# Kernel optimization log

Measured on AMD Instinct MI355X. Metric: run time of the kernel, lower is better.

Reference implementation:

```python
import jax, jax.numpy as jnp
import numpy as np

HIDDEN = 1024
EMB = HIDDEN // 2          # embedding_dim = hidden_dim // 2
NUM_OPS = 8
BATCH = 16384


def setup_inputs() -> dict:
    key = jax.random.key(0)
    ks = jax.random.split(key, 8)
    x = jax.random.normal(ks[0], (BATCH, HIDDEN), dtype=jnp.float32)
    sampled_ops = jax.random.randint(ks[1], (BATCH,), 0, NUM_OPS, dtype=jnp.int32)
    op_emb = jax.random.normal(ks[2], (NUM_OPS, EMB), dtype=jnp.float32) * 0.02
    # per-expert 2-layer MLP params (Linear stored as [in, out] for x @ W)
    s1 = 1.0 / np.sqrt(HIDDEN + EMB)
    s2 = 1.0 / np.sqrt(HIDDEN)
    W1 = jax.random.uniform(ks[3], (NUM_OPS, HIDDEN + EMB, HIDDEN), jnp.float32, -s1, s1)
    b1 = jax.random.uniform(ks[4], (NUM_OPS, HIDDEN), jnp.float32, -s1, s1)
    W2 = jax.random.uniform(ks[5], (NUM_OPS, HIDDEN, HIDDEN), jnp.float32, -s2, s2)
    b2 = jax.random.uniform(ks[6], (NUM_OPS, HIDDEN), jnp.float32, -s2, s2)
    return {"x": x, "sampled_ops": sampled_ops, "op_emb": op_emb,
            "W1": W1, "b1": b1, "W2": W2, "b2": b2}


def reference(x, sampled_ops, op_emb, W1, b1, W2, b2):
    # gather per-token operator embedding and augment input
    emb = jnp.take(op_emb, sampled_ops, axis=0)            # [B, EMB]
    x_aug = jnp.concatenate([x, emb], axis=-1)             # [B, H+EMB]
    num_ops = W1.shape[0]
    out = jnp.zeros_like(x)
    # loop over the small fixed expert set; mask-combine per token
    for o in range(num_ops):
        h = jax.nn.relu(x_aug @ W1[o] + b1[o])             # [B, H]
        y = jax.nn.relu(h @ W2[o] + b2[o])                 # [B, H]
        mask = (sampled_ops == o)[:, None]
        out = out + jnp.where(mask, y, 0.0)
    return out
```

## Files before the change

kernel.cpp:

```cpp
#include <hip/hip_runtime.h>
#include <hip/hip_bf16.h>

#define BATCH 16384
#define HID   1024
#define EMBD  512
#define NOPS  8
#define MAXT  136
#define CNTS  16

typedef __attribute__((ext_vector_type(8))) short bf16x8;
typedef __attribute__((ext_vector_type(4))) float f32x4;

__device__ __forceinline__ unsigned short f2bf(float f) {
  unsigned int u = __float_as_uint(f);
  u += 0x7FFF + ((u >> 16) & 1);
  return (unsigned short)(u >> 16);
}

__device__ __forceinline__ unsigned int pk2(float a, float b) {
  __hip_bfloat162 t = __float22bfloat162_rn(make_float2(a, b));
  return *(unsigned int*)(&t);
}

__device__ __forceinline__ void lds_load16(void* lds, const void* g) {
  __builtin_amdgcn_global_load_lds(
      (const __attribute__((address_space(1))) unsigned int*)g,
      (__attribute__((address_space(3))) unsigned int*)lds, 16, 0, 0);
}

__device__ __forceinline__ void decode_bid(int bid, int& g, int& nx) {
  g = 17 * (bid & 7) + (bid >> 6);
  nx = (bid >> 3) & 7;
}

__device__ __forceinline__ void w_prep_tile(const float* __restrict__ W,
                                            short* __restrict__ Wp,
                                            int ks, int nx, int tid) {
  int n = tid & 127, kh = tid >> 7;
  const float* src = W + (size_t)(ks * 32 + kh * 16) * 1024 + nx * 128 + n;
  float v[16];
#pragma unroll
  for (int kk = 0; kk < 16; ++kk) v[kk] = src[(size_t)kk * 1024];
  uint4 a, b;
  a.x = pk2(v[0], v[1]);  a.y = pk2(v[2], v[3]);
  a.z = pk2(v[4], v[5]);  a.w = pk2(v[6], v[7]);
  b.x = pk2(v[8], v[9]);  b.y = pk2(v[10], v[11]);
  b.z = pk2(v[12], v[13]); b.w = pk2(v[14], v[15]);
  uint4* dst = (uint4*)(Wp + (size_t)n * 32);
  dst[kh * 2] = a;
  dst[kh * 2 + 1] = b;
}

__global__ void bucket_w1_k(const int* __restrict__ ops, int* __restrict__ cnt,
                            int* __restrict__ idx, const float* __restrict__ W1,
                            short* __restrict__ W1p) {
  int bid = blockIdx.x;
  int tid = threadIdx.x;
  if (bid >= 64) {
    int b = bid - 64;
    int e = b / 384; int r = b % 384; int nx = r / 48, ks = r % 48;
    w_prep_tile(W1 + (size_t)e * 1536 * 1024,
                W1p + ((size_t)(e * 8 + nx) * 48 + ks) * 4096, ks, nx, tid);
    return;
  }
  __shared__ int wcnt[4][NOPS];
  __shared__ int wbase[4][NOPS];
  int lane = tid & 63, w = tid >> 6;
  int t = bid * 256 + tid;
  int op = ops[t];
  unsigned long long msave = 0;
#pragma unroll
  for (int o = 0; o < NOPS; ++o) {
    unsigned long long mm = __ballot(op == o);
    if (op == o) msave = mm;
    if (lane == o) wcnt[w][o] = __popcll(mm);
  }
  __syncthreads();
  if (tid < NOPS) {
    int c0 = wcnt[0][tid], c1 = wcnt[1][tid], c2 = wcnt[2][tid], c3 = wcnt[3][tid];
    int base = atomicAdd(&cnt[tid * CNTS], c0 + c1 + c2 + c3);
    wbase[0][tid] = base;
    wbase[1][tid] = base + c0;
    wbase[2][tid] = base + c0 + c1;
    wbase[3][tid] = base + c0 + c1 + c2;
  }
  __syncthreads();
  int pre = __popcll(msave & ((1ull << lane) - 1ull));
  idx[op * BATCH + wbase[w][op] + pre] = t;
}

__global__ void schedule_k(const int* __restrict__ cnt, int* __restrict__ desc,
                           int* __restrict__ ntp, int* __restrict__ idx) {
  if (threadIdx.x == 0) {
    int n = 0;
    for (int e = 0; e < NOPS; ++e) {
      int c = cnt[e * CNTS];
      for (int t = 0; t < c; t += 128) { desc[2 * n] = e; desc[2 * n + 1] = t; ++n; }
    }
    *ntp = n;
  }
  for (int e = 0; e < NOPS; ++e) {
    int c = cnt[e * CNTS];
    int cp = (c + 127) & ~127;
    for (int p = c + (int)threadIdx.x; p < cp; p += 256) idx[e * BATCH + p] = 0;
  }
}

__global__ void prep_a_k(const float* __restrict__ x, const float* __restrict__ emb,
                         const int* __restrict__ idx, const int* __restrict__ desc,
                         const int* __restrict__ ntp, short* __restrict__ Ap) {
  __shared__ int toks[128];
  int bid = blockIdx.x;
  int g = bid / 12, kx = bid % 12;
  if (g >= *ntp) return;
  int e = desc[2 * g], rs = desc[2 * g + 1];
  int tid = threadIdx.x;
  if (tid < 128) toks[tid] = idx[e * BATCH + rs + tid];
  __syncthreads();
  int r = tid >> 1, ah = tid & 1;
  int tok = toks[r];
  short* dst0 = Ap + (size_t)g * 48 * 4096;
#pragma unroll
  for (int kk = 0; kk < 4; ++kk) {
    int ks = kx * 4 + kk;
    const float* src = (ks < 32) ? (x + (size_t)tok * HID + ks * 32 + ah * 16)
                                 : (emb + e * EMBD + (ks - 32) * 32 + ah * 16);
    float4 f0 = ((const float4*)src)[0];
    float4 f1 = ((const float4*)src)[1];
    float4 f2v = ((const float4*)src)[2];
    float4 f3 = ((const float4*)src)[3];
    uint4 p0 = make_uint4(pk2(f0.x, f0.y), pk2(f0.z, f0.w), pk2(f1.x, f1.y), pk2(f1.z, f1.w));
    uint4 p1 = make_uint4(pk2(f2v.x, f2v.y), pk2(f2v.z, f2v.w), pk2(f3.x, f3.y), pk2(f3.z, f3.w));
    short* dst = dst0 + ks * 4096 + r * 32 + ah * 16;
    ((uint4*)dst)[0] = p0;
    ((uint4*)dst)[1] = p1;
  }
}

__global__ __launch_bounds__(256) void gemm1_w2_k(
    const short* __restrict__ Ap, const float* __restrict__ b1,
    const short* __restrict__ W1p, unsigned short* __restrict__ hp,
    const int* __restrict__ desc, const int* __restrict__ ntp,
    const float* __restrict__ W2, short* __restrict__ W2p) {
  int bid = blockIdx.x;
  int tid = threadIdx.x;
  if (bid >= 8 * MAXT) {
    int b = bid - 8 * MAXT;
    int e = b / 256; int r = b % 256; int nx = r / 32, ks = r % 32;
    w_prep_tile(W2 + (size_t)e * 1024 * 1024,
                W2p + ((size_t)(e * 8 + nx) * 32 + ks) * 4096, ks, nx, tid);
    return;
  }
  int g, nx;
  decode_bid(bid, g, nx);
  if (g >= *ntp) return;
  int e = desc[2 * g];

  __shared__ __align__(16) char smem[16384];
  short* lA = (short*)smem;
  short* lB = (short*)(smem + 8192);

  int lane = tid & 63, w = tid >> 6;
  int wm = w >> 1, wn = w & 1;
  int fr = lane & 15, fq = lane >> 4;

  const char* Asrc = (const char*)Ap + (size_t)g * 48 * 8192;
  const char* Bsrc = (const char*)W1p + (size_t)(e * 8 + nx) * 48 * 8192;

  f32x4 acc[4][4] = {};

  for (int ks = 0; ks < 48; ++ks) {
    const char* as = Asrc + ks * 8192;
    const char* bs = Bsrc + ks * 8192;
    lds_load16(smem + w * 1024, as + w * 1024 + lane * 16);
    lds_load16(smem + 4096 + w * 1024, as + 4096 + w * 1024 + lane * 16);
    lds_load16(smem + 8192 + w * 1024, bs + w * 1024 + lane * 16);
    lds_load16(smem + 12288 + w * 1024, bs + 4096 + w * 1024 + lane * 16);
    __syncthreads();

    bf16x8 af[4], bfr[4];
#pragma unroll
    for (int i = 0; i < 4; ++i)
      af[i] = *(const bf16x8*)&lA[(wm * 64 + i * 16 + fr) * 32 + fq * 8];
#pragma unroll
    for (int j = 0; j < 4; ++j)
      bfr[j] = *(const bf16x8*)&lB[(wn * 64 + j * 16 + fr) * 32 + fq * 8];
#pragma unroll
    for (int i = 0; i < 4; ++i)
#pragma unroll
      for (int j = 0; j < 4; ++j)
        acc[i][j] = __builtin_amdgcn_mfma_f32_16x16x32_bf16(af[i], bfr[j], acc[i][j], 0, 0, 0);
    __syncthreads();
  }

  float bias[4];
#pragma unroll
  for (int j = 0; j < 4; ++j)
    bias[j] = b1[e * HID + nx * 128 + wn * 64 + j * 16 + fr];

  unsigned short* ls = (unsigned short*)smem;
  int lr = lane >> 2;
#pragma unroll
  for (int i = 0; i < 4; ++i) {
    __syncthreads();
#pragma unroll
    for (int j = 0; j < 4; ++j)
#pragma unroll
      for (int rg = 0; rg < 4; ++rg) {
        float v = acc[i][j][rg] + bias[j];
        v = v > 0.f ? v : 0.f;
        ls[w * 1024 + (fq * 4 + rg) * 64 + j * 16 + fr] = f2bf(v);
      }
    __syncthreads();
    int R = wm * 64 + i * 16 + lr;
#pragma unroll
    for (int s = 0; s < 2; ++s) {
      int ch = (lane & 3) + s * 4;
      int ks2 = nx * 4 + wn * 2 + (ch >> 2);
      uint4 val = *(const uint4*)&ls[w * 1024 + lr * 64 + ch * 8];
      *(uint4*)(hp + ((size_t)(g * 32 + ks2) * 128 + R) * 32 + (ch & 3) * 8) = val;
    }
  }
}

__global__ __launch_bounds__(256) void gemm2_k(
    const unsigned short* __restrict__ hp, const float* __restrict__ b2,
    const short* __restrict__ W2p, float* __restrict__ out,
    const int* __restrict__ idx, const int* __restrict__ cnt,
    const int* __restrict__ desc, const int* __restrict__ ntp) {
  int g, nx;
  decode_bid(blockIdx.x, g, nx);
  if (g >= *ntp) return;
  int e = desc[2 * g], rs = desc[2 * g + 1];
  int ce = cnt[e * CNTS];

  __shared__ __align__(16) char smem[16384];
  __shared__ int toks[128];
  short* lA = (short*)smem;
  short* lB = (short*)(smem + 8192);

  int tid = threadIdx.x, lane = tid & 63, w = tid >> 6;
  int wm = w >> 1, wn = w & 1;
  int fr = lane & 15, fq = lane >> 4;

  if (tid < 128) toks[tid] = idx[e * BATCH + rs + tid];

  const char* Asrc = (const char*)hp + (size_t)g * 32 * 8192;
  const char* Bsrc = (const char*)W2p + (size_t)(e * 8 + nx) * 32 * 8192;

  f32x4 acc[4][4] = {};

  for (int ks = 0; ks < 32; ++ks) {
    const char* as = Asrc + ks * 8192;
    const char* bs = Bsrc + ks * 8192;
    lds_load16(smem + w * 1024, as + w * 1024 + lane * 16);
    lds_load16(smem + 4096 + w * 1024, as + 4096 + w * 1024 + lane * 16);
    lds_load16(smem + 8192 + w * 1024, bs + w * 1024 + lane * 16);
    lds_load16(smem + 12288 + w * 1024, bs + 4096 + w * 1024 + lane * 16);
    __syncthreads();

    bf16x8 af[4], bfr[4];
#pragma unroll
    for (int i = 0; i < 4; ++i)
      af[i] = *(const bf16x8*)&lA[(wm * 64 + i * 16 + fr) * 32 + fq * 8];
#pragma unroll
    for (int j = 0; j < 4; ++j)
      bfr[j] = *(const bf16x8*)&lB[(wn * 64 + j * 16 + fr) * 32 + fq * 8];
#pragma unroll
    for (int i = 0; i < 4; ++i)
#pragma unroll
      for (int j = 0; j < 4; ++j)
        acc[i][j] = __builtin_amdgcn_mfma_f32_16x16x32_bf16(af[i], bfr[j], acc[i][j], 0, 0, 0);
    __syncthreads();
  }

  float bias[4];
#pragma unroll
  for (int j = 0; j < 4; ++j)
    bias[j] = b2[e * HID + nx * 128 + wn * 64 + j * 16 + fr];

  float* lsf = (float*)smem;
  int lr = lane >> 2;
#pragma unroll
  for (int i = 0; i < 4; ++i) {
    __syncthreads();
#pragma unroll
    for (int j = 0; j < 4; ++j)
#pragma unroll
      for (int rg = 0; rg < 4; ++rg) {
        float v = acc[i][j][rg] + bias[j];
        lsf[w * 1024 + (fq * 4 + rg) * 64 + j * 16 + fr] = v > 0.f ? v : 0.f;
      }
    __syncthreads();
    int R = wm * 64 + i * 16 + lr;
    if (R < ce - rs) {
      float* orow = out + (size_t)toks[R] * HID + nx * 128 + wn * 64;
#pragma unroll
      for (int s = 0; s < 4; ++s) {
        int ch = (lane & 3) + s * 4;
        *(float4*)(orow + ch * 4) = *(const float4*)&lsf[w * 1024 + lr * 64 + ch * 4];
      }
    }
  }
}


extern "C" void kernel_launch(void* const* d_in, const int* in_sizes, int n_in,
                              void* d_out, int out_size, void* d_ws, size_t ws_size,
                              hipStream_t stream) {
  const float* x   = (const float*)d_in[0];
  const int*   ops = (const int*)d_in[1];
  const float* emb = (const float*)d_in[2];
  const float* W1  = (const float*)d_in[3];
  const float* b1  = (const float*)d_in[4];
  const float* W2  = (const float*)d_in[5];
  const float* b2  = (const float*)d_in[6];
  float* out = (float*)d_out;

  char* ws = (char*)d_ws;
  int* cnt  = (int*)(ws + 0);
  int* ntp  = (int*)(ws + 1024);
  int* desc = (int*)(ws + 1280);
  int* idx  = (int*)(ws + 4096);
  short* W1p = (short*)(ws + 528384);
  short* W2p = (short*)(ws + 25694208);
  unsigned short* hp = (unsigned short*)(ws + 42471424);
  short* Ap = (short*)(ws + 78123008);

  hipMemsetAsync(cnt, 0, 512, stream);
  bucket_w1_k<<<64 + 3072, 256, 0, stream>>>(ops, cnt, idx, W1, W1p);
  schedule_k<<<1, 256, 0, stream>>>(cnt, desc, ntp, idx);
  prep_a_k<<<12 * MAXT, 256, 0, stream>>>(x, emb, idx, desc, ntp, Ap);
  gemm1_w2_k<<<8 * MAXT + 2048, 256, 0, stream>>>(Ap, b1, W1p, hp, desc, ntp, W2, W2p);
  gemm2_k<<<8 * MAXT, 256, 0, stream>>>(hp, b2, W2p, out, idx, cnt, desc, ntp);
}
```

Before: 325.0 us.

## Fold per-expert embedding contribution into a precomputed first-layer bias

```diff
diff --git a/kernel.cpp b/kernel.cpp
--- a/kernel.cpp
+++ b/kernel.cpp
@@ -53,14 +53,30 @@
 
 __global__ void bucket_w1_k(const int* __restrict__ ops, int* __restrict__ cnt,
                             int* __restrict__ idx, const float* __restrict__ W1,
-                            short* __restrict__ W1p) {
+                            short* __restrict__ W1p, const float* __restrict__ emb,
+                            const float* __restrict__ b1, float* __restrict__ ce) {
   int bid = blockIdx.x;
   int tid = threadIdx.x;
-  if (bid >= 64) {
+  if (bid >= 64 && bid < 64 + 2048) {
     int b = bid - 64;
-    int e = b / 384; int r = b % 384; int nx = r / 48, ks = r % 48;
+    int e = b / 256; int r = b % 256; int nx = r / 32, ks = r % 32;
     w_prep_tile(W1 + (size_t)e * 1536 * 1024,
-                W1p + ((size_t)(e * 8 + nx) * 48 + ks) * 4096, ks, nx, tid);
+                W1p + ((size_t)(e * 8 + nx) * 32 + ks) * 4096, ks, nx, tid);
+    return;
+  }
+  if (bid >= 64 + 2048) {
+    __shared__ float se[EMBD];
+    int b2 = bid - 64 - 2048;
+    int e = b2 >> 2, part = b2 & 3;
+    int n = part * 256 + tid;
+    se[tid] = emb[e * EMBD + tid];
+    se[tid + 256] = emb[e * EMBD + tid + 256];
+    __syncthreads();
+    const float* Wc = W1 + (size_t)e * 1536 * 1024 + (size_t)1024 * 1024 + n;
+    float acc = b1[e * HID + n];
+#pragma unroll 8
+    for (int k = 0; k < EMBD; ++k) acc += se[k] * Wc[(size_t)k * 1024];
+    ce[e * HID + n] = acc;
     return;
   }
   __shared__ int wcnt[4][NOPS];
@@ -106,12 +122,12 @@
   }
 }
 
-__global__ void prep_a_k(const float* __restrict__ x, const float* __restrict__ emb,
+__global__ void prep_a_k(const float* __restrict__ x,
                          const int* __restrict__ idx, const int* __restrict__ desc,
                          const int* __restrict__ ntp, short* __restrict__ Ap) {
   __shared__ int toks[128];
   int bid = blockIdx.x;
-  int g = bid / 12, kx = bid % 12;
+  int g = bid >> 3, kx = bid & 7;
   if (g >= *ntp) return;
   int e = desc[2 * g], rs = desc[2 * g + 1];
   int tid = threadIdx.x;
@@ -119,12 +135,11 @@
   __syncthreads();
   int r = tid >> 1, ah = tid & 1;
   int tok = toks[r];
-  short* dst0 = Ap + (size_t)g * 48 * 4096;
+  short* dst0 = Ap + (size_t)g * 32 * 4096;
 #pragma unroll
   for (int kk = 0; kk < 4; ++kk) {
     int ks = kx * 4 + kk;
-    const float* src = (ks < 32) ? (x + (size_t)tok * HID + ks * 32 + ah * 16)
-                                 : (emb + e * EMBD + (ks - 32) * 32 + ah * 16);
+    const float* src = x + (size_t)tok * HID + ks * 32 + ah * 16;
     float4 f0 = ((const float4*)src)[0];
     float4 f1 = ((const float4*)src)[1];
     float4 f2v = ((const float4*)src)[2];
@@ -138,7 +153,7 @@
 }
 
 __global__ __launch_bounds__(256) void gemm1_w2_k(
-    const short* __restrict__ Ap, const float* __restrict__ b1,
+    const short* __restrict__ Ap, const float* __restrict__ ce,
     const short* __restrict__ W1p, unsigned short* __restrict__ hp,
     const int* __restrict__ desc, const int* __restrict__ ntp,
     const float* __restrict__ W2, short* __restrict__ W2p) {
@@ -164,12 +179,12 @@
   int wm = w >> 1, wn = w & 1;
   int fr = lane & 15, fq = lane >> 4;
 
-  const char* Asrc = (const char*)Ap + (size_t)g * 48 * 8192;
-  const char* Bsrc = (const char*)W1p + (size_t)(e * 8 + nx) * 48 * 8192;
+  const char* Asrc = (const char*)Ap + (size_t)g * 32 * 8192;
+  const char* Bsrc = (const char*)W1p + (size_t)(e * 8 + nx) * 32 * 8192;
 
   f32x4 acc[4][4] = {};
 
-  for (int ks = 0; ks < 48; ++ks) {
+  for (int ks = 0; ks < 32; ++ks) {
     const char* as = Asrc + ks * 8192;
     const char* bs = Bsrc + ks * 8192;
     lds_load16(smem + w * 1024, as + w * 1024 + lane * 16);
@@ -196,7 +211,7 @@
   float bias[4];
 #pragma unroll
   for (int j = 0; j < 4; ++j)
-    bias[j] = b1[e * HID + nx * 128 + wn * 64 + j * 16 + fr];
+    bias[j] = ce[e * HID + nx * 128 + wn * 64 + j * 16 + fr];
 
   unsigned short* ls = (unsigned short*)smem;
   int lr = lane >> 2;
@@ -232,7 +247,7 @@
   decode_bid(blockIdx.x, g, nx);
   if (g >= *ntp) return;
   int e = desc[2 * g], rs = desc[2 * g + 1];
-  int ce = cnt[e * CNTS];
+  int ce2 = cnt[e * CNTS];
 
   __shared__ __align__(16) char smem[16384];
   __shared__ int toks[128];
@@ -293,7 +308,7 @@
       }
     __syncthreads();
     int R = wm * 64 + i * 16 + lr;
-    if (R < ce - rs) {
+    if (R < ce2 - rs) {
       float* orow = out + (size_t)toks[R] * HID + nx * 128 + wn * 64;
 #pragma unroll
       for (int s = 0; s < 4; ++s) {
@@ -323,14 +338,15 @@
   int* desc = (int*)(ws + 1280);
   int* idx  = (int*)(ws + 4096);
   short* W1p = (short*)(ws + 528384);
-  short* W2p = (short*)(ws + 25694208);
-  unsigned short* hp = (unsigned short*)(ws + 42471424);
-  short* Ap = (short*)(ws + 78123008);
+  short* W2p = (short*)(ws + 17305600);
+  float* ce  = (float*)(ws + 34082816);
+  unsigned short* hp = (unsigned short*)(ws + 34115584);
+  short* Ap = (short*)(ws + 69767168);
 
   hipMemsetAsync(cnt, 0, 512, stream);
-  bucket_w1_k<<<64 + 3072, 256, 0, stream>>>(ops, cnt, idx, W1, W1p);
+  bucket_w1_k<<<64 + 2048 + 32, 256, 0, stream>>>(ops, cnt, idx, W1, W1p, emb, b1, ce);
   schedule_k<<<1, 256, 0, stream>>>(cnt, desc, ntp, idx);
-  prep_a_k<<<12 * MAXT, 256, 0, stream>>>(x, emb, idx, desc, ntp, Ap);
-  gemm1_w2_k<<<8 * MAXT + 2048, 256, 0, stream>>>(Ap, b1, W1p, hp, desc, ntp, W2, W2p);
+  prep_a_k<<<8 * MAXT, 256, 0, stream>>>(x, idx, desc, ntp, Ap);
+  gemm1_w2_k<<<8 * MAXT + 2048, 256, 0, stream>>>(Ap, ce, W1p, hp, desc, ntp, W2, W2p);
   gemm2_k<<<8 * MAXT, 256, 0, stream>>>(hp, b2, W2p, out, idx, cnt, desc, ntp);
 }
```

Result: slower. 340.0 us (+4.6%).
